# Kernel tuning notes

Measured on AMD Instinct MI355X. Metric: run time of the kernel, lower is better.

Reference implementation:

```python
import jax, jax.numpy as jnp
import numpy as np

VOCAB, EMBED, HIDDEN, N_CLASSES = 50257, 128, 256, 2
B = S = 512  # must be equal: the original module only runs when x.size(0)==x.size(1)


def gru_layer(x_seq, Wih, Whh, bih, bhh):
    """PyTorch-equation GRU over time axis 0. x_seq: (T, N, E) -> (T, N, H)."""
    T, N, _ = x_seq.shape
    H = Whh.shape[1]
    xi = x_seq @ Wih.T + bih  # precompute input projections for all steps: (T, N, 3H)

    def step(h, xi_t):
        gh = h @ Whh.T + bhh
        xr, xz, xn = jnp.split(xi_t, 3, axis=-1)
        hr, hz, hn = jnp.split(gh, 3, axis=-1)
        r = jax.nn.sigmoid(xr + hr)
        z = jax.nn.sigmoid(xz + hz)
        n = jnp.tanh(xn + r * hn)
        h_new = (1.0 - z) * n + z * h
        return h_new, h_new

    h0 = jnp.zeros((N, H), dtype=x_seq.dtype)
    _, ys = jax.lax.scan(step, h0, xi)
    return ys


def setup_inputs() -> dict:
    key = jax.random.key(0)
    ks = jax.random.split(key, 12)
    sc = 0.05
    return {
        "x": jax.random.randint(ks[0], (B, S), 0, VOCAB),
        "embed_table": jax.random.normal(ks[1], (VOCAB, EMBED), jnp.float32) * sc,
        "Wih0": jax.random.normal(ks[2], (3 * HIDDEN, EMBED), jnp.float32) * sc,
        "Whh0": jax.random.normal(ks[3], (3 * HIDDEN, HIDDEN), jnp.float32) * sc,
        "bih0": jax.random.normal(ks[4], (3 * HIDDEN,), jnp.float32) * sc,
        "bhh0": jax.random.normal(ks[5], (3 * HIDDEN,), jnp.float32) * sc,
        "Wih1": jax.random.normal(ks[6], (3 * HIDDEN, HIDDEN), jnp.float32) * sc,
        "Whh1": jax.random.normal(ks[7], (3 * HIDDEN, HIDDEN), jnp.float32) * sc,
        "bih1": jax.random.normal(ks[8], (3 * HIDDEN,), jnp.float32) * sc,
        "bhh1": jax.random.normal(ks[9], (3 * HIDDEN,), jnp.float32) * sc,
        "W_out": jax.random.normal(ks[10], (N_CLASSES, HIDDEN), jnp.float32) * sc,
        "b_out": jax.random.normal(ks[11], (N_CLASSES,), jnp.float32) * sc,
    }


def reference(x, embed_table, Wih0, Whh0, bih0, bhh0, Wih1, Whh1, bih1, bhh1, W_out, b_out):
    emb = embed_table[x]                 # (B, S, E)
    # nn.GRU default batch_first=False: dim 0 (=B) is TIME, dim 1 (=S) is batch.
    y = gru_layer(emb, Wih0, Whh0, bih0, bhh0)   # (B, S, H)
    y = gru_layer(y, Wih1, Whh1, bih1, bhh1)     # (B, S, H)
    h_t = y[:, -1, :]                    # (B, H)
    # self.dropout(h_t) in the original discards its result -> no-op.
    logit = h_t @ W_out.T + b_out        # (B, n_classes)
    return logit
```

## Files before the change

kernel.cpp:

```cpp
#include <hip/hip_runtime.h>
#include <hip/hip_fp16.h>

typedef _Float16 f16x2 __attribute__((ext_vector_type(2)));
typedef _Float16 half8 __attribute__((ext_vector_type(8)));

#define TS  512
#define HID 256
#define G3  768
#define EMB 128
#define THR 512
#define NB1 12
#define RPB 64
#define CTL 511
#define BSZ 8

__device__ __forceinline__ float sigmoidf_(float x){ return 1.0f/(1.0f+__expf(-x)); }
__device__ __forceinline__ float tanhf_(float x){
  float e = __expf(-2.0f*fabsf(x));
  float t = (1.0f-e)/(1.0f+e);
  return copysignf(t,x);
}

__global__ __launch_bounds__(256) void xi0_kernel(const int* __restrict__ x,
    const float* __restrict__ emb_tab, const float* __restrict__ Wih0,
    const float* __restrict__ bih0, float* __restrict__ xi0,
    const float* __restrict__ Whh0, const float* __restrict__ Whh1,
    _Float16* __restrict__ wpk0, _Float16* __restrict__ wpk1)
{
  __shared__ float embs[8][EMB];
  __shared__ int idx8[8];
  int tid = threadIdx.x;
  int t0  = blockIdx.x * 8;
  if (tid < 8) idx8[tid] = x[(t0 + tid)*512 + 511];
  __syncthreads();
  for (int i = tid; i < 8*EMB; i += 256){
    int q = i >> 7, r = i & 127;
    embs[q][r] = emb_tab[(long)idx8[q]*EMB + r];
  }
  __syncthreads();
  for (int g = 0; g < 3; g++){
    int j = g*256 + tid;
    float b = bih0[j];
    float acc[8];
    #pragma unroll
    for (int u=0;u<8;u++) acc[u]=b;
    const float4* wrow = (const float4*)(Wih0 + (long)j*EMB);
    #pragma unroll 8
    for (int m=0;m<EMB/4;m++){
      float4 w = wrow[m];
      #pragma unroll
      for (int u=0;u<8;u++){
        acc[u] += w.x*embs[u][4*m+0] + w.y*embs[u][4*m+1]
                + w.z*embs[u][4*m+2] + w.w*embs[u][4*m+3];
      }
    }
    #pragma unroll
    for (int u=0;u<8;u++) xi0[(long)(t0+u)*G3 + j] = acc[u];
  }
  int gid = blockIdx.x*256 + tid;
  for (int e = gid; e < 2*192*256; e += 64*256){
    int L = (e >= 192*256) ? 1 : 0;
    int i = e - L*192*256;
    int s = i >> 8, c = i & 255;
    int row = 12*(s/3) + 9 + (s%3);
    const float* W = L ? Whh1 : Whh0;
    _Float16*    P = L ? wpk1 : wpk0;
    P[i] = (_Float16)W[(long)row*HID + c];
  }
}

#define SHUF(V,A,B) __builtin_shufflevector(V,V,A,B)
#define WR24(X) X(0,0) X(0,1) X(0,2) X(0,3) X(1,0) X(1,1) X(1,2) X(1,3) \
                X(2,0) X(2,1) X(2,2) X(2,3) X(3,0) X(3,1) X(3,2) X(3,3) \
                X(4,0) X(4,1) X(4,2) X(4,3) X(5,0) X(5,1) X(5,2) X(5,3)

template<int MODE>
__device__ __forceinline__ void rec_layer(const float* __restrict__ Whh,
    const float* __restrict__ bhh, const float* __restrict__ xi,
    const _Float16* __restrict__ wpk,
    _Float16* __restrict__ h16out, float* __restrict__ f32out,
    unsigned* __restrict__ flagB, unsigned* __restrict__ cntB,
    _Float16 (*hbuf)[8*40], half8* ldsw, float* gh, float* bhhL)
{
  int tid = threadIdx.x;
  int g   = tid >> 3;
  int o   = tid & 7;

#define WDECL(I,C) half8 w##I##_##C;
  WR24(WDECL)
#define WLOAD(I,C) { \
    const float4* p_ = (const float4*)(Whh + (long)(12*g+(I))*HID + 32*o + 8*(C)); \
    float4 u_ = p_[0], v_ = p_[1]; \
    w##I##_##C = (half8){(_Float16)u_.x,(_Float16)u_.y,(_Float16)u_.z,(_Float16)u_.w, \
                         (_Float16)v_.x,(_Float16)v_.y,(_Float16)v_.z,(_Float16)v_.w}; }
  WR24(WLOAD)

  #pragma unroll
  for (int k = 0; k < 12; k++){
    int row = 12*g + 6 + (k >> 2);
    int C = k & 3;
    const float4* p_ = (const float4*)(Whh + (long)row*HID + 32*o + 8*C);
    float4 u_ = p_[0], v_ = p_[1];
    ldsw[k*THR + tid] = (half8){(_Float16)u_.x,(_Float16)u_.y,(_Float16)u_.z,(_Float16)u_.w,
                                (_Float16)v_.x,(_Float16)v_.y,(_Float16)v_.z,(_Float16)v_.w};
  }
  const half8* sp0 = (const half8*)(wpk + ((long)(3*g+0))*HID + 32*o);
  const half8* sp1 = (const half8*)(wpk + ((long)(3*g+1))*HID + 32*o);
  const half8* sp2 = (const half8*)(wpk + ((long)(3*g+2))*HID + 32*o);

  float hprev = 0.f;
  float xr=0.f, xz=0.f, xn=0.f;
  for (int i = tid; i < G3; i += THR) bhhL[i] = bhh[i];
  if (tid < 80) ((half8*)hbuf)[tid] = (half8)(_Float16)0;

  if (MODE == 1 && tid == CTL){
    while (__hip_atomic_load(&cntB[0], __ATOMIC_RELAXED, __HIP_MEMORY_SCOPE_AGENT) < NB1)
      __builtin_amdgcn_s_sleep(1);
    __threadfence();
  }
  __syncthreads();
  if (tid < HID){
    xr = xi[tid]; xz = xi[HID+tid]; xn = xi[2*HID+tid];
  }

  for (int t = 0; t < TS; t++){
    if (MODE == 1 && tid == CTL && ((t+1) & (BSZ-1)) == 0 && t+1 < TS){
      unsigned b = (unsigned)(t+1) >> 3;
      while (__hip_atomic_load(&cntB[b], __ATOMIC_RELAXED, __HIP_MEMORY_SCOPE_AGENT) < NB1)
        __builtin_amdgcn_s_sleep(1);
      __threadfence();
    }

    const half8* hp = (const half8*)(&hbuf[t & 1][o*40]);
    float a0=0.f,a1=0.f,a2=0.f,a3=0.f,a4=0.f,a5=0.f,
          a6=0.f,a7=0.f,a8=0.f,a9=0.f,a10=0.f,a11=0.f;
#define D8(ACC, WV, HV) \
    ACC = __builtin_amdgcn_fdot2(SHUF(WV,0,1), SHUF(HV,0,1), ACC, false); \
    ACC = __builtin_amdgcn_fdot2(SHUF(WV,2,3), SHUF(HV,2,3), ACC, false); \
    ACC = __builtin_amdgcn_fdot2(SHUF(WV,4,5), SHUF(HV,4,5), ACC, false); \
    ACC = __builtin_amdgcn_fdot2(SHUF(WV,6,7), SHUF(HV,6,7), ACC, false);
#define CHUNK(C) { half8 hv = hp[C]; \
    half8 l0 = ldsw[(0*4+(C))*THR + tid]; \
    half8 l1 = ldsw[(1*4+(C))*THR + tid]; \
    half8 l2 = ldsw[(2*4+(C))*THR + tid]; \
    half8 s0 = sp0[C]; half8 s1 = sp1[C]; half8 s2 = sp2[C]; \
    D8(a0, w0_##C, hv) D8(a1, w1_##C, hv) D8(a2, w2_##C, hv) \
    D8(a3, w3_##C, hv) D8(a4, w4_##C, hv) D8(a5, w5_##C, hv) \
    D8(a6, l0, hv) D8(a7, l1, hv) D8(a8, l2, hv) \
    D8(a9, s0, hv) D8(a10, s1, hv) D8(a11, s2, hv) }
    CHUNK(0) CHUNK(1) CHUNK(2) CHUNK(3)

    bool b0 = o & 1, b1 = o & 2, b2 = o & 4;
    float s, r_;
    s = b0 ? a0 : a1; r_ = __shfl_xor(s, 1, 64); float c0 = (b0 ? a1 : a0) + r_;
    s = b0 ? a2 : a3; r_ = __shfl_xor(s, 1, 64); float c1 = (b0 ? a3 : a2) + r_;
    s = b0 ? a4 : a5; r_ = __shfl_xor(s, 1, 64); float c2 = (b0 ? a5 : a4) + r_;
    s = b0 ? a6 : a7; r_ = __shfl_xor(s, 1, 64); float c3 = (b0 ? a7 : a6) + r_;
    s = b1 ? c0 : c1; r_ = __shfl_xor(s, 2, 64); float d0 = (b1 ? c1 : c0) + r_;
    s = b1 ? c2 : c3; r_ = __shfl_xor(s, 2, 64); float d1 = (b1 ? c3 : c2) + r_;
    s = b2 ? d0 : d1; r_ = __shfl_xor(s, 4, 64); float e  = (b2 ? d1 : d0) + r_;
    gh[12*g + o] = e;
    s = b0 ? a8 : a9;   r_ = __shfl_xor(s, 1, 64); float c4 = (b0 ? a9  : a8 ) + r_;
    s = b0 ? a10 : a11; r_ = __shfl_xor(s, 1, 64); float c5 = (b0 ? a11 : a10) + r_;
    s = b1 ? c4 : c5;   r_ = __shfl_xor(s, 2, 64); float d2 = (b1 ? c5  : c4 ) + r_;
    float e2 = d2 + __shfl_xor(d2, 4, 64);
    if (o < 4) gh[12*g + 8 + o] = e2;
    __syncthreads();

    if (tid < HID){
      float r = sigmoidf_(xr + bhhL[tid] + gh[tid]);
      float z = sigmoidf_(xz + bhhL[HID+tid] + gh[HID+tid]);
      float n = tanhf_(xn + r*(gh[2*HID+tid] + bhhL[2*HID+tid]));
      float hnew = (1.0f - z)*n + z*hprev;
      hprev = hnew;
      if (MODE == 1) f32out[(long)t*HID + tid] = hnew;
      float partner = __shfl_xor(hnew, 1, 64);
      if ((tid & 1) == 0){
        f16x2 p; p.x = (_Float16)hnew; p.y = (_Float16)partner;
        *(f16x2*)(&hbuf[(t+1)&1][(tid>>5)*40 + (tid&31)]) = p;
        if (MODE == 0) *(f16x2*)(h16out + (long)t*HID + tid) = p;
      }
      if (t+1 < TS){
        const float* xp = xi + (long)(t+1)*G3;
        xr = xp[tid]; xz = xp[HID+tid]; xn = xp[2*HID+tid];
      }
    }
    __syncthreads();
    if (MODE == 0 && tid == CTL && ((t+1) & (BSZ-1)) == 0){
      __threadfence();
      __hip_atomic_store(&flagB[t >> 3], 1u, __ATOMIC_RELEASE, __HIP_MEMORY_SCOPE_AGENT);
    }
  }
}

__device__ __forceinline__ void xi1_stage(const float* __restrict__ Wih1,
    const float* __restrict__ bih1, const _Float16* __restrict__ h16,
    float* __restrict__ xi1, unsigned* __restrict__ flagB,
    unsigned* __restrict__ cntB, int slice)
{
  int tid = threadIdx.x;
  int r = tid >> 3, o = tid & 7;
  int row = slice*RPB + r;
  half8 w0,w1,w2,w3;
  {
    const float4* wp = (const float4*)(Wih1 + (long)row*HID + o*32);
    float4 p0=wp[0],p1=wp[1],p2=wp[2],p3=wp[3],p4=wp[4],p5=wp[5],p6=wp[6],p7=wp[7];
    w0 = (half8){(_Float16)p0.x,(_Float16)p0.y,(_Float16)p0.z,(_Float16)p0.w,
                 (_Float16)p1.x,(_Float16)p1.y,(_Float16)p1.z,(_Float16)p1.w};
    w1 = (half8){(_Float16)p2.x,(_Float16)p2.y,(_Float16)p2.z,(_Float16)p2.w,
                 (_Float16)p3.x,(_Float16)p3.y,(_Float16)p3.z,(_Float16)p3.w};
    w2 = (half8){(_Float16)p4.x,(_Float16)p4.y,(_Float16)p4.z,(_Float16)p4.w,
                 (_Float16)p5.x,(_Float16)p5.y,(_Float16)p5.z,(_Float16)p5.w};
    w3 = (half8){(_Float16)p6.x,(_Float16)p6.y,(_Float16)p6.z,(_Float16)p6.w,
                 (_Float16)p7.x,(_Float16)p7.y,(_Float16)p7.z,(_Float16)p7.w};
  }
  float bias = bih1[row];

  for (int b = 0; b < TS/BSZ; b++){
    if (tid == 0){
      while (__hip_atomic_load(&flagB[b], __ATOMIC_RELAXED, __HIP_MEMORY_SCOPE_AGENT) == 0u)
        __builtin_amdgcn_s_sleep(1);
      __threadfence();
    }
    __syncthreads();
    #pragma unroll 4
    for (int u = 0; u < BSZ; u++){
      int t = b*BSZ + u;
      const half8* hp = (const half8*)(h16 + (long)t*HID + o*32);
      half8 h0 = hp[0], h1 = hp[1], h2 = hp[2], h3 = hp[3];
      float acc = 0.f;
#define XDOT(W,H) \
      acc = __builtin_amdgcn_fdot2(SHUF(W,0,1), SHUF(H,0,1), acc, false); \
      acc = __builtin_amdgcn_fdot2(SHUF(W,2,3), SHUF(H,2,3), acc, false); \
      acc = __builtin_amdgcn_fdot2(SHUF(W,4,5), SHUF(H,4,5), acc, false); \
      acc = __builtin_amdgcn_fdot2(SHUF(W,6,7), SHUF(H,6,7), acc, false);
      XDOT(w0,h0) XDOT(w1,h1) XDOT(w2,h2) XDOT(w3,h3)
      acc += __shfl_xor(acc, 1, 64);
      acc += __shfl_xor(acc, 2, 64);
      acc += __shfl_xor(acc, 4, 64);
      if (o == 0) xi1[(long)t*G3 + row] = acc + bias;
    }
    __syncthreads();
    if (tid == 0){
      __threadfence();
      atomicAdd(&cntB[b], 1u);
    }
  }
}

__global__ __launch_bounds__(THR, 2)
void pipe_kernel(
    const float* __restrict__ Whh0, const float* __restrict__ bhh0,
    const float* __restrict__ xi0,
    const float* __restrict__ Wih1, const float* __restrict__ bih1,
    const float* __restrict__ Whh1, const float* __restrict__ bhh1,
    const _Float16* __restrict__ wpk0, const _Float16* __restrict__ wpk1,
    _Float16* __restrict__ h1f16, float* __restrict__ xi1,
    float* __restrict__ h2, unsigned* __restrict__ flagB,
    unsigned* __restrict__ cntB)
{
  __shared__ __align__(16) half8 ldsw[12*THR];
  __shared__ __align__(16) _Float16 hbuf[2][8*40];
  __shared__ float gh[G3];
  __shared__ float bhhL[G3];
  int bid = blockIdx.x;
  if (bid == 0)
    rec_layer<0>(Whh0, bhh0, xi0, wpk0, h1f16, nullptr, flagB, cntB, hbuf, ldsw, gh, bhhL);
  else if (bid == 13)
    rec_layer<1>(Whh1, bhh1, xi1, wpk1, nullptr, h2, flagB, cntB, hbuf, ldsw, gh, bhhL);
  else
    xi1_stage(Wih1, bih1, h1f16, xi1, flagB, cntB, bid - 1);
}

__global__ __launch_bounds__(1024) void logits_kernel(const float* __restrict__ h2,
    const float* __restrict__ Wout, const float* __restrict__ bout,
    float* __restrict__ out)
{
  __shared__ __align__(16) float wsm[2*HID];
  __shared__ float bs[2];
  int tid = threadIdx.x;
  if (tid < 2*HID) wsm[tid] = Wout[tid];
  if (tid < 2)     bs[tid]  = bout[tid];
  __syncthreads();
  int t = tid >> 1, c = tid & 1;
  const float4* hr = (const float4*)(h2 + (long)t*HID);
  const float4* wr = (const float4*)(wsm + c*HID);
  float acc = bs[c];
  #pragma unroll 8
  for (int m=0;m<HID/4;m++){
    float4 h = hr[m]; float4 wv = wr[m];
    acc += h.x*wv.x + h.y*wv.y + h.z*wv.z + h.w*wv.w;
  }
  out[tid] = acc;
}

extern "C" void kernel_launch(void* const* d_in, const int* in_sizes, int n_in,
                              void* d_out, int out_size, void* d_ws, size_t ws_size,
                              hipStream_t stream)
{
  const int*   x    = (const int*)  d_in[0];
  const float* emb  = (const float*)d_in[1];
  const float* Wih0 = (const float*)d_in[2];
  const float* Whh0 = (const float*)d_in[3];
  const float* bih0 = (const float*)d_in[4];
  const float* bhh0 = (const float*)d_in[5];
  const float* Wih1 = (const float*)d_in[6];
  const float* Whh1 = (const float*)d_in[7];
  const float* bih1 = (const float*)d_in[8];
  const float* bhh1 = (const float*)d_in[9];
  const float* Wout = (const float*)d_in[10];
  const float* bout = (const float*)d_in[11];
  float* out = (float*)d_out;

  char* ws = (char*)d_ws;
  float*     xi0   = (float*)(ws);
  float*     xi1   = (float*)(ws + 1572864);
  _Float16*  h1f16 = (_Float16*)(ws + 3145728);
  float*     h2    = (float*)(ws + 3407872);
  unsigned*  flagB = (unsigned*)(ws + 3932160);
  unsigned*  cntB  = (unsigned*)(ws + 3934208);
  _Float16*  wpk0  = (_Float16*)(ws + 3936256);
  _Float16*  wpk1  = (_Float16*)(ws + 4034560);

  hipMemsetAsync(ws + 3932160, 0, 4096, stream);
  xi0_kernel<<<64, 256, 0, stream>>>(x, emb, Wih0, bih0, xi0,
                                     Whh0, Whh1, wpk0, wpk1);
  pipe_kernel<<<14, THR, 0, stream>>>(Whh0, bhh0, xi0, Wih1, bih1,
                                      Whh1, bhh1, wpk0, wpk1,
                                      h1f16, xi1, h2, flagB, cntB);
  logits_kernel<<<1, 1024, 0, stream>>>(h2, Wout, bout, out);
}
```

Measured before the change: 893.7 us.

## Halve recurrent block to 256 threads with 24 rows per thread group

The recurrent GRU blocks drop from 512 to 256 threads. Each 8-thread group now covers 24 weight rows instead of 12: 12 rows held in registers, 9 in LDS (36 half8 slots per thread) and 3 read from a global packed copy. The xi1 stage computes two rows per thread to match the smaller block, and launch bounds drop to one block per CU. The goal is cheaper per-step barriers and a single warp-group reduction tree, at the cost of twice the fdot2 work per thread on the serial critical path and much higher register and LDS pressure, with a risk of spills.

```diff
diff --git a/kernel.cpp b/kernel.cpp
--- a/kernel.cpp
+++ b/kernel.cpp
@@ -8,10 +8,10 @@
 #define HID 256
 #define G3  768
 #define EMB 128
-#define THR 512
+#define THR 256
 #define NB1 12
 #define RPB 64
-#define CTL 511
+#define CTL 255
 #define BSZ 8
 
 __device__ __forceinline__ float sigmoidf_(float x){ return 1.0f/(1.0f+__expf(-x)); }
@@ -58,11 +58,11 @@
     for (int u=0;u<8;u++) xi0[(long)(t0+u)*G3 + j] = acc[u];
   }
   int gid = blockIdx.x*256 + tid;
-  for (int e = gid; e < 2*192*256; e += 64*256){
-    int L = (e >= 192*256) ? 1 : 0;
-    int i = e - L*192*256;
+  for (int e = gid; e < 2*96*256; e += 64*256){
+    int L = (e >= 96*256) ? 1 : 0;
+    int i = e - L*96*256;
     int s = i >> 8, c = i & 255;
-    int row = 12*(s/3) + 9 + (s%3);
+    int row = 24*(s/3) + 21 + (s%3);
     const float* W = L ? Whh1 : Whh0;
     _Float16*    P = L ? wpk1 : wpk0;
     P[i] = (_Float16)W[(long)row*HID + c];
@@ -70,9 +70,40 @@
 }
 
 #define SHUF(V,A,B) __builtin_shufflevector(V,V,A,B)
-#define WR24(X) X(0,0) X(0,1) X(0,2) X(0,3) X(1,0) X(1,1) X(1,2) X(1,3) \
+#define WR48(X) X(0,0) X(0,1) X(0,2) X(0,3) X(1,0) X(1,1) X(1,2) X(1,3) \
                 X(2,0) X(2,1) X(2,2) X(2,3) X(3,0) X(3,1) X(3,2) X(3,3) \
-                X(4,0) X(4,1) X(4,2) X(4,3) X(5,0) X(5,1) X(5,2) X(5,3)
+                X(4,0) X(4,1) X(4,2) X(4,3) X(5,0) X(5,1) X(5,2) X(5,3) \
+                X(6,0) X(6,1) X(6,2) X(6,3) X(7,0) X(7,1) X(7,2) X(7,3) \
+                X(8,0) X(8,1) X(8,2) X(8,3) X(9,0) X(9,1) X(9,2) X(9,3) \
+                X(10,0) X(10,1) X(10,2) X(10,3) X(11,0) X(11,1) X(11,2) X(11,3)
+
+#define D8(ACC, WV, HV) \
+    ACC = __builtin_amdgcn_fdot2(SHUF(WV,0,1), SHUF(HV,0,1), ACC, false); \
+    ACC = __builtin_amdgcn_fdot2(SHUF(WV,2,3), SHUF(HV,2,3), ACC, false); \
+    ACC = __builtin_amdgcn_fdot2(SHUF(WV,4,5), SHUF(HV,4,5), ACC, false); \
+    ACC = __builtin_amdgcn_fdot2(SHUF(WV,6,7), SHUF(HV,6,7), ACC, false);
+
+#define RD(ACC, I) \
+    D8(ACC, w##I##_0, hv0) D8(ACC, w##I##_1, hv1) \
+    D8(ACC, w##I##_2, hv2) D8(ACC, w##I##_3, hv3)
+
+#define LROW(ACC, K) { \
+    half8 l0_ = ldsw[((K)*4+0)*THR + tid]; \
+    half8 l1_ = ldsw[((K)*4+1)*THR + tid]; \
+    half8 l2_ = ldsw[((K)*4+2)*THR + tid]; \
+    half8 l3_ = ldsw[((K)*4+3)*THR + tid]; \
+    D8(ACC, l0_, hv0) D8(ACC, l1_, hv1) D8(ACC, l2_, hv2) D8(ACC, l3_, hv3) }
+
+#define TREE(x0,x1,x2,x3,x4,x5,x6,x7, BASE) { \
+    float s_, r2_; \
+    s_ = b0 ? x0 : x1; r2_ = __shfl_xor(s_,1,64); float t0_ = (b0 ? x1 : x0) + r2_; \
+    s_ = b0 ? x2 : x3; r2_ = __shfl_xor(s_,1,64); float t1_ = (b0 ? x3 : x2) + r2_; \
+    s_ = b0 ? x4 : x5; r2_ = __shfl_xor(s_,1,64); float t2_ = (b0 ? x5 : x4) + r2_; \
+    s_ = b0 ? x6 : x7; r2_ = __shfl_xor(s_,1,64); float t3_ = (b0 ? x7 : x6) + r2_; \
+    s_ = b1 ? t0_ : t1_; r2_ = __shfl_xor(s_,2,64); float u0_ = (b1 ? t1_ : t0_) + r2_; \
+    s_ = b1 ? t2_ : t3_; r2_ = __shfl_xor(s_,2,64); float u1_ = (b1 ? t3_ : t2_) + r2_; \
+    s_ = b2 ? u0_ : u1_; r2_ = __shfl_xor(s_,4,64); float v_  = (b2 ? u1_ : u0_) + r2_; \
+    gh[24*g + (BASE) + o] = v_; }
 
 template<int MODE>
 __device__ __forceinline__ void rec_layer(const float* __restrict__ Whh,
@@ -87,26 +118,26 @@
   int o   = tid & 7;
 
 #define WDECL(I,C) half8 w##I##_##C;
-  WR24(WDECL)
+  WR48(WDECL)
 #define WLOAD(I,C) { \
-    const float4* p_ = (const float4*)(Whh + (long)(12*g+(I))*HID + 32*o + 8*(C)); \
+    const float4* p_ = (const float4*)(Whh + (long)(24*g+(I))*HID + 32*o + 8*(C)); \
     float4 u_ = p_[0], v_ = p_[1]; \
     w##I##_##C = (half8){(_Float16)u_.x,(_Float16)u_.y,(_Float16)u_.z,(_Float16)u_.w, \
                          (_Float16)v_.x,(_Float16)v_.y,(_Float16)v_.z,(_Float16)v_.w}; }
-  WR24(WLOAD)
+  WR48(WLOAD)
 
   #pragma unroll
-  for (int k = 0; k < 12; k++){
-    int row = 12*g + 6 + (k >> 2);
+  for (int k = 0; k < 36; k++){
+    int row = 24*g + 12 + (k >> 2);
     int C = k & 3;
     const float4* p_ = (const float4*)(Whh + (long)row*HID + 32*o + 8*C);
     float4 u_ = p_[0], v_ = p_[1];
     ldsw[k*THR + tid] = (half8){(_Float16)u_.x,(_Float16)u_.y,(_Float16)u_.z,(_Float16)u_.w,
                                 (_Float16)v_.x,(_Float16)v_.y,(_Float16)v_.z,(_Float16)v_.w};
   }
-  const half8* sp0 = (const half8*)(wpk + ((long)(3*g+0))*HID + 32*o);
-  const half8* sp1 = (const half8*)(wpk + ((long)(3*g+1))*HID + 32*o);
-  const half8* sp2 = (const half8*)(wpk + ((long)(3*g+2))*HID + 32*o);
+  const half8* spA = (const half8*)(wpk + ((long)(3*g+0))*HID + 32*o);
+  const half8* spB = (const half8*)(wpk + ((long)(3*g+1))*HID + 32*o);
+  const half8* spC = (const half8*)(wpk + ((long)(3*g+2))*HID + 32*o);
 
   float hprev = 0.f;
   float xr=0.f, xz=0.f, xn=0.f;
@@ -119,9 +150,7 @@
     __threadfence();
   }
   __syncthreads();
-  if (tid < HID){
-    xr = xi[tid]; xz = xi[HID+tid]; xn = xi[2*HID+tid];
-  }
+  xr = xi[tid]; xz = xi[HID+tid]; xn = xi[2*HID+tid];
 
   for (int t = 0; t < TS; t++){
     if (MODE == 1 && tid == CTL && ((t+1) & (BSZ-1)) == 0 && t+1 < TS){
@@ -132,42 +161,30 @@
     }
 
     const half8* hp = (const half8*)(&hbuf[t & 1][o*40]);
+    half8 hv0 = hp[0], hv1 = hp[1], hv2 = hp[2], hv3 = hp[3];
     float a0=0.f,a1=0.f,a2=0.f,a3=0.f,a4=0.f,a5=0.f,
-          a6=0.f,a7=0.f,a8=0.f,a9=0.f,a10=0.f,a11=0.f;
-#define D8(ACC, WV, HV) \
-    ACC = __builtin_amdgcn_fdot2(SHUF(WV,0,1), SHUF(HV,0,1), ACC, false); \
-    ACC = __builtin_amdgcn_fdot2(SHUF(WV,2,3), SHUF(HV,2,3), ACC, false); \
-    ACC = __builtin_amdgcn_fdot2(SHUF(WV,4,5), SHUF(HV,4,5), ACC, false); \
-    ACC = __builtin_amdgcn_fdot2(SHUF(WV,6,7), SHUF(HV,6,7), ACC, false);
-#define CHUNK(C) { half8 hv = hp[C]; \
-    half8 l0 = ldsw[(0*4+(C))*THR + tid]; \
-    half8 l1 = ldsw[(1*4+(C))*THR + tid]; \
-    half8 l2 = ldsw[(2*4+(C))*THR + tid]; \
-    half8 s0 = sp0[C]; half8 s1 = sp1[C]; half8 s2 = sp2[C]; \
-    D8(a0, w0_##C, hv) D8(a1, w1_##C, hv) D8(a2, w2_##C, hv) \
-    D8(a3, w3_##C, hv) D8(a4, w4_##C, hv) D8(a5, w5_##C, hv) \
-    D8(a6, l0, hv) D8(a7, l1, hv) D8(a8, l2, hv) \
-    D8(a9, s0, hv) D8(a10, s1, hv) D8(a11, s2, hv) }
-    CHUNK(0) CHUNK(1) CHUNK(2) CHUNK(3)
+          a6=0.f,a7=0.f,a8=0.f,a9=0.f,a10=0.f,a11=0.f,
+          a12=0.f,a13=0.f,a14=0.f,a15=0.f,a16=0.f,a17=0.f,
+          a18=0.f,a19=0.f,a20=0.f,a21=0.f,a22=0.f,a23=0.f;
+
+    half8 sA0 = spA[0], sA1 = spA[1], sA2 = spA[2], sA3 = spA[3];
+    RD(a0,0) RD(a1,1) RD(a2,2) RD(a3,3) RD(a4,4) RD(a5,5)
+    D8(a21, sA0, hv0) D8(a21, sA1, hv1) D8(a21, sA2, hv2) D8(a21, sA3, hv3)
+    half8 sB0 = spB[0], sB1 = spB[1], sB2 = spB[2], sB3 = spB[3];
+    RD(a6,6) RD(a7,7) RD(a8,8) RD(a9,9) RD(a10,10) RD(a11,11)
+    D8(a22, sB0, hv0) D8(a22, sB1, hv1) D8(a22, sB2, hv2) D8(a22, sB3, hv3)
+    half8 sC0 = spC[0], sC1 = spC[1], sC2 = spC[2], sC3 = spC[3];
+    LROW(a12,0) LROW(a13,1) LROW(a14,2) LROW(a15,3) LROW(a16,4)
+    LROW(a17,5) LROW(a18,6) LROW(a19,7) LROW(a20,8)
+    D8(a23, sC0, hv0) D8(a23, sC1, hv1) D8(a23, sC2, hv2) D8(a23, sC3, hv3)
 
     bool b0 = o & 1, b1 = o & 2, b2 = o & 4;
-    float s, r_;
-    s = b0 ? a0 : a1; r_ = __shfl_xor(s, 1, 64); float c0 = (b0 ? a1 : a0) + r_;
-    s = b0 ? a2 : a3; r_ = __shfl_xor(s, 1, 64); float c1 = (b0 ? a3 : a2) + r_;
-    s = b0 ? a4 : a5; r_ = __shfl_xor(s, 1, 64); float c2 = (b0 ? a5 : a4) + r_;
-    s = b0 ? a6 : a7; r_ = __shfl_xor(s, 1, 64); float c3 = (b0 ? a7 : a6) + r_;
-    s = b1 ? c0 : c1; r_ = __shfl_xor(s, 2, 64); float d0 = (b1 ? c1 : c0) + r_;
-    s = b1 ? c2 : c3; r_ = __shfl_xor(s, 2, 64); float d1 = (b1 ? c3 : c2) + r_;
-    s = b2 ? d0 : d1; r_ = __shfl_xor(s, 4, 64); float e  = (b2 ? d1 : d0) + r_;
-    gh[12*g + o] = e;
-    s = b0 ? a8 : a9;   r_ = __shfl_xor(s, 1, 64); float c4 = (b0 ? a9  : a8 ) + r_;
-    s = b0 ? a10 : a11; r_ = __shfl_xor(s, 1, 64); float c5 = (b0 ? a11 : a10) + r_;
-    s = b1 ? c4 : c5;   r_ = __shfl_xor(s, 2, 64); float d2 = (b1 ? c5  : c4 ) + r_;
-    float e2 = d2 + __shfl_xor(d2, 4, 64);
-    if (o < 4) gh[12*g + 8 + o] = e2;
+    TREE(a0,a1,a2,a3,a4,a5,a6,a7, 0)
+    TREE(a8,a9,a10,a11,a12,a13,a14,a15, 8)
+    TREE(a16,a17,a18,a19,a20,a21,a22,a23, 16)
     __syncthreads();
 
-    if (tid < HID){
+    {
       float r = sigmoidf_(xr + bhhL[tid] + gh[tid]);
       float z = sigmoidf_(xz + bhhL[HID+tid] + gh[HID+tid]);
       float n = tanhf_(xn + r*(gh[2*HID+tid] + bhhL[2*HID+tid]));
@@ -200,21 +217,35 @@
 {
   int tid = threadIdx.x;
   int r = tid >> 3, o = tid & 7;
-  int row = slice*RPB + r;
-  half8 w0,w1,w2,w3;
+  int rowA = slice*RPB + r;
+  int rowB = rowA + 32;
+  half8 wa0,wa1,wa2,wa3, wb0,wb1,wb2,wb3;
   {
-    const float4* wp = (const float4*)(Wih1 + (long)row*HID + o*32);
+    const float4* wp = (const float4*)(Wih1 + (long)rowA*HID + o*32);
     float4 p0=wp[0],p1=wp[1],p2=wp[2],p3=wp[3],p4=wp[4],p5=wp[5],p6=wp[6],p7=wp[7];
-    w0 = (half8){(_Float16)p0.x,(_Float16)p0.y,(_Float16)p0.z,(_Float16)p0.w,
-                 (_Float16)p1.x,(_Float16)p1.y,(_Float16)p1.z,(_Float16)p1.w};
-    w1 = (half8){(_Float16)p2.x,(_Float16)p2.y,(_Float16)p2.z,(_Float16)p2.w,
-                 (_Float16)p3.x,(_Float16)p3.y,(_Float16)p3.z,(_Float16)p3.w};
-    w2 = (half8){(_Float16)p4.x,(_Float16)p4.y,(_Float16)p4.z,(_Float16)p4.w,
-                 (_Float16)p5.x,(_Float16)p5.y,(_Float16)p5.z,(_Float16)p5.w};
-    w3 = (half8){(_Float16)p6.x,(_Float16)p6.y,(_Float16)p6.z,(_Float16)p6.w,
-                 (_Float16)p7.x,(_Float16)p7.y,(_Float16)p7.z,(_Float16)p7.w};
-  }
-  float bias = bih1[row];
+    wa0 = (half8){(_Float16)p0.x,(_Float16)p0.y,(_Float16)p0.z,(_Float16)p0.w,
+                  (_Float16)p1.x,(_Float16)p1.y,(_Float16)p1.z,(_Float16)p1.w};
+    wa1 = (half8){(_Float16)p2.x,(_Float16)p2.y,(_Float16)p2.z,(_Float16)p2.w,
+                  (_Float16)p3.x,(_Float16)p3.y,(_Float16)p3.z,(_Float16)p3.w};
+    wa2 = (half8){(_Float16)p4.x,(_Float16)p4.y,(_Float16)p4.z,(_Float16)p4.w,
+                  (_Float16)p5.x,(_Float16)p5.y,(_Float16)p5.z,(_Float16)p5.w};
+    wa3 = (half8){(_Float16)p6.x,(_Float16)p6.y,(_Float16)p6.z,(_Float16)p6.w,
+                  (_Float16)p7.x,(_Float16)p7.y,(_Float16)p7.z,(_Float16)p7.w};
+  }
+  {
+    const float4* wp = (const float4*)(Wih1 + (long)rowB*HID + o*32);
+    float4 p0=wp[0],p1=wp[1],p2=wp[2],p3=wp[3],p4=wp[4],p5=wp[5],p6=wp[6],p7=wp[7];
+    wb0 = (half8){(_Float16)p0.x,(_Float16)p0.y,(_Float16)p0.z,(_Float16)p0.w,
+                  (_Float16)p1.x,(_Float16)p1.y,(_Float16)p1.z,(_Float16)p1.w};
+    wb1 = (half8){(_Float16)p2.x,(_Float16)p2.y,(_Float16)p2.z,(_Float16)p2.w,
+                  (_Float16)p3.x,(_Float16)p3.y,(_Float16)p3.z,(_Float16)p3.w};
+    wb2 = (half8){(_Float16)p4.x,(_Float16)p4.y,(_Float16)p4.z,(_Float16)p4.w,
+                  (_Float16)p5.x,(_Float16)p5.y,(_Float16)p5.z,(_Float16)p5.w};
+    wb3 = (half8){(_Float16)p6.x,(_Float16)p6.y,(_Float16)p6.z,(_Float16)p6.w,
+                  (_Float16)p7.x,(_Float16)p7.y,(_Float16)p7.z,(_Float16)p7.w};
+  }
+  float biasA = bih1[rowA];
+  float biasB = bih1[rowB];
 
   for (int b = 0; b < TS/BSZ; b++){
     if (tid == 0){
@@ -223,22 +254,24 @@
       __threadfence();
     }
     __syncthreads();
-    #pragma unroll 4
+    #pragma unroll 2
     for (int u = 0; u < BSZ; u++){
       int t = b*BSZ + u;
       const half8* hp = (const half8*)(h16 + (long)t*HID + o*32);
       half8 h0 = hp[0], h1 = hp[1], h2 = hp[2], h3 = hp[3];
-      float acc = 0.f;
-#define XDOT(W,H) \
-      acc = __builtin_amdgcn_fdot2(SHUF(W,0,1), SHUF(H,0,1), acc, false); \
-      acc = __builtin_amdgcn_fdot2(SHUF(W,2,3), SHUF(H,2,3), acc, false); \
-      acc = __builtin_amdgcn_fdot2(SHUF(W,4,5), SHUF(H,4,5), acc, false); \
-      acc = __builtin_amdgcn_fdot2(SHUF(W,6,7), SHUF(H,6,7), acc, false);
-      XDOT(w0,h0) XDOT(w1,h1) XDOT(w2,h2) XDOT(w3,h3)
-      acc += __shfl_xor(acc, 1, 64);
-      acc += __shfl_xor(acc, 2, 64);
-      acc += __shfl_xor(acc, 4, 64);
-      if (o == 0) xi1[(long)t*G3 + row] = acc + bias;
+      float accA = 0.f, accB = 0.f;
+      D8(accA, wa0, h0) D8(accA, wa1, h1) D8(accA, wa2, h2) D8(accA, wa3, h3)
+      D8(accB, wb0, h0) D8(accB, wb1, h1) D8(accB, wb2, h2) D8(accB, wb3, h3)
+      accA += __shfl_xor(accA, 1, 64);
+      accA += __shfl_xor(accA, 2, 64);
+      accA += __shfl_xor(accA, 4, 64);
+      accB += __shfl_xor(accB, 1, 64);
+      accB += __shfl_xor(accB, 2, 64);
+      accB += __shfl_xor(accB, 4, 64);
+      if (o == 0){
+        xi1[(long)t*G3 + rowA] = accA + biasA;
+        xi1[(long)t*G3 + rowB] = accB + biasB;
+      }
     }
     __syncthreads();
     if (tid == 0){
@@ -248,7 +281,7 @@
   }
 }
 
-__global__ __launch_bounds__(THR, 2)
+__global__ __launch_bounds__(THR, 1)
 void pipe_kernel(
     const float* __restrict__ Whh0, const float* __restrict__ bhh0,
     const float* __restrict__ xi0,
@@ -259,7 +292,7 @@
     float* __restrict__ h2, unsigned* __restrict__ flagB,
     unsigned* __restrict__ cntB)
 {
-  __shared__ __align__(16) half8 ldsw[12*THR];
+  __shared__ __align__(16) half8 ldsw[36*THR];
   __shared__ __align__(16) _Float16 hbuf[2][8*40];
   __shared__ float gh[G3];
   __shared__ float bhhL[G3];
@@ -320,7 +353,7 @@
   unsigned*  flagB = (unsigned*)(ws + 3932160);
   unsigned*  cntB  = (unsigned*)(ws + 3934208);
   _Float16*  wpk0  = (_Float16*)(ws + 3936256);
-  _Float16*  wpk1  = (_Float16*)(ws + 4034560);
+  _Float16*  wpk1  = (_Float16*)(ws + 3985408);
 
   hipMemsetAsync(ws + 3932160, 0, 4096, stream);
   xi0_kernel<<<64, 256, 0, stream>>>(x, emb, Wih0, bih0, xi0,
```

New measurement: 1.559 ms. +74.4%, slower.
